# Optimization experiments

Hardware: AMD Instinct MI355X
Metric: run time of the kernel (lower is better)

Reference implementation:

```python
import jax, jax.numpy as jnp
import numpy as np

B, S, D, H = 4, 2048, 1024, 16
HD = D // H
ROPE_THETA = 10000.0


def setup_inputs() -> dict:
    key = jax.random.key(0)
    ks = jax.random.split(key, 5)
    scale = 1.0 / np.sqrt(D)
    inp = {
        "x": jax.random.normal(ks[0], (B, S, D), dtype=jnp.float32),
        "Wq": jax.random.normal(ks[1], (D, D), dtype=jnp.float32) * scale,
        "bq": jnp.zeros((D,), jnp.float32),
        "Wk": jax.random.normal(ks[2], (D, D), dtype=jnp.float32) * scale,
        "bk": jnp.zeros((D,), jnp.float32),
        "Wv": jax.random.normal(ks[3], (D, D), dtype=jnp.float32) * scale,
        "bv": jnp.zeros((D,), jnp.float32),
        "Wo": jax.random.normal(ks[4], (D, D), dtype=jnp.float32) * scale,
        "bo": jnp.zeros((D,), jnp.float32),
        # causal mask: True means masked (j > i), matching masked_fill semantics
        "attn_mask": jnp.triu(jnp.ones((S, S), dtype=bool), k=1),
    }
    return inp


def _rope(x):
    # x: [B, H, S, HD]; half-split rotary embedding
    half = HD // 2
    inv_freq = 1.0 / (ROPE_THETA ** (jnp.arange(0, half, dtype=jnp.float32) / half))
    pos = jnp.arange(x.shape[2], dtype=jnp.float32)
    freqs = pos[:, None] * inv_freq[None, :]            # [S, half]
    cos = jnp.cos(freqs)[None, None]                    # [1,1,S,half]
    sin = jnp.sin(freqs)[None, None]
    x1, x2 = x[..., :half], x[..., half:]
    return jnp.concatenate([x1 * cos - x2 * sin, x2 * cos + x1 * sin], axis=-1)


def reference(x, Wq, bq, Wk, bk, Wv, bv, Wo, bo, attn_mask):
    def shape(t):  # [B,S,D] -> [B,H,S,HD]
        return t.reshape(B, S, H, HD).transpose(0, 2, 1, 3)

    q = shape(x @ Wq.T + bq)
    k = shape(x @ Wk.T + bk)
    v = shape(x @ Wv.T + bv)
    q = _rope(q)
    k = _rope(k)
    scores = jnp.einsum("bhqd,bhkd->bhqk", q, k) * (HD ** -0.5)
    scores = jnp.where(attn_mask[None, None], -jnp.inf, scores)
    w = jax.nn.softmax(scores, axis=-1)
    attn = jnp.einsum("bhqk,bhkd->bhqd", w, v)
    merged = attn.transpose(0, 2, 1, 3).reshape(B, S, D)
    return merged @ Wo.T + bo
```

## Files before the change

### kernel.cpp

```cpp
#include <hip/hip_runtime.h>
#include <math.h>

#define BATCH 4
#define SEQ   2048
#define DMODEL 1024
#define NHEAD 16
#define HDIM  64
#define MROWS (BATCH*SEQ)

typedef unsigned short u16;
typedef unsigned int   u32;

using bf16x8 = __attribute__((ext_vector_type(8))) short;
using f32x4  = __attribute__((ext_vector_type(4))) float;
using f32x16 = __attribute__((ext_vector_type(16))) float;

__device__ __forceinline__ u16 f2bf(float f) {
    u32 u = __float_as_uint(f);
    u += 0x7fffu + ((u >> 16) & 1u);
    return (u16)(u >> 16);
}
__device__ __forceinline__ u32 pack2bf(float a, float b) {
    u32 ua = __float_as_uint(a); ua += 0x7fffu + ((ua >> 16) & 1u);
    u32 ub = __float_as_uint(b); ub += 0x7fffu + ((ub >> 16) & 1u);
    return (ua >> 16) | (ub & 0xffff0000u);
}

#define GLOBAL_LOAD_LDS16(gp, lp)                                              \
    __builtin_amdgcn_global_load_lds(                                          \
        (const __attribute__((address_space(1))) void*)(gp),                   \
        (__attribute__((address_space(3))) void*)(lp), 16, 0, 0)

__global__ __launch_bounds__(256) void convert_inputs(
    const float* __restrict__ x,  const float* __restrict__ wq,
    const float* __restrict__ wk, const float* __restrict__ wv,
    const float* __restrict__ wo, u16* __restrict__ dst)
{
    long long i4 = ((long long)blockIdx.x * 256 + threadIdx.x) * 4;
    const float* src; long long off;
    if (i4 < 8388608LL) { src = x; off = i4; }
    else {
        long long j = i4 - 8388608LL;
        int seg = (int)(j >> 20);
        off = j & 1048575LL;
        src = (seg == 0) ? wq : (seg == 1) ? wk : (seg == 2) ? wv : wo;
    }
    float4 v = *(const float4*)(src + off);
    u32 lo = (u32)f2bf(v.x) | ((u32)f2bf(v.y) << 16);
    u32 hi = (u32)f2bf(v.z) | ((u32)f2bf(v.w) << 16);
    *(uint2*)(dst + i4) = make_uint2(lo, hi);
}

template<int QKV>
__global__ __launch_bounds__(256) void gemm_mfma(
    const u16* __restrict__ A,
    const u16* __restrict__ Wq_, const u16* __restrict__ Wk_, const u16* __restrict__ Wv_,
    const float* __restrict__ bq_, const float* __restrict__ bk_, const float* __restrict__ bv_,
    u16* __restrict__ Cq_, u16* __restrict__ Ck_, u16* __restrict__ Cv_,
    float* __restrict__ Cf)
{
    __shared__ u16 As[128 * 32];
    __shared__ u16 Ws[128 * 32];

    const int t    = threadIdx.x;
    const int lane = t & 63;
    const int w    = t >> 6;
    const int quad = lane >> 4;
    const int l15  = lane & 15;

    const int bx  = blockIdx.x;
    const int xcd = bx & 7;
    const int i_  = bx >> 3;
    const int bml = i_ & 7;
    const int n_  = (QKV ? ((i_ >> 3) & 7) : (i_ >> 3));
    const int seg = (QKV ? (i_ >> 6) : 0);

    const u16*   W    = (seg == 0) ? Wq_ : (seg == 1) ? Wk_ : Wv_;
    const float* bias = (seg == 0) ? bq_ : (seg == 1) ? bk_ : bv_;
    u16*         Cb   = (seg == 0) ? Cq_ : (seg == 1) ? Ck_ : Cv_;

    const int bm   = (xcd * 8 + bml) * 128;
    const int bn   = n_ * 128;
    const int wrow = (w & 1) * 64;
    const int wcol = (w >> 1) * 64;

    const int srl = lane >> 2;
    const int sc  = (lane & 3) ^ ((lane >> 3) & 3);

    f32x4 acc[4][4] = {};

    for (int k0 = 0; k0 < DMODEL; k0 += 32) {
        __syncthreads();
        #pragma unroll
        for (int i = 0; i < 2; i++) {
            int row = 32 * w + 16 * i + srl;
            GLOBAL_LOAD_LDS16(A + (size_t)(bm + row) * DMODEL + k0 + sc * 8,
                              &As[(32 * w + 16 * i) * 32]);
            GLOBAL_LOAD_LDS16(W + (size_t)(bn + row) * DMODEL + k0 + sc * 8,
                              &Ws[(32 * w + 16 * i) * 32]);
        }
        __syncthreads();

        bf16x8 af[4], bfr[4];
        const int pc = quad ^ ((l15 >> 1) & 3);
        #pragma unroll
        for (int i = 0; i < 4; i++)
            af[i] = *(const bf16x8*)&As[(wrow + 16 * i + l15) * 32 + pc * 8];
        #pragma unroll
        for (int j = 0; j < 4; j++)
            bfr[j] = *(const bf16x8*)&Ws[(wcol + 16 * j + l15) * 32 + pc * 8];
        #pragma unroll
        for (int i = 0; i < 4; i++)
            #pragma unroll
            for (int j = 0; j < 4; j++)
                acc[i][j] = __builtin_amdgcn_mfma_f32_16x16x32_bf16(af[i], bfr[j], acc[i][j], 0, 0, 0);
    }

    float bv[4];
    #pragma unroll
    for (int j = 0; j < 4; j++) bv[j] = bias[bn + wcol + 16 * j + l15];

    if constexpr (QKV == 0) {
        #pragma unroll
        for (int i = 0; i < 4; i++)
            #pragma unroll
            for (int r = 0; r < 4; r++) {
                int mg = bm + wrow + 16 * i + quad * 4 + r;
                #pragma unroll
                for (int j = 0; j < 4; j++)
                    Cf[(size_t)mg * DMODEL + bn + wcol + 16 * j + l15] = acc[i][j][r] + bv[j];
            }
    } else {
        if (seg == 2) {
            #pragma unroll
            for (int i = 0; i < 4; i++)
                #pragma unroll
                for (int r = 0; r < 4; r++) {
                    int mg = bm + wrow + 16 * i + quad * 4 + r;
                    #pragma unroll
                    for (int j = 0; j < 4; j++)
                        Cb[(size_t)mg * DMODEL + bn + wcol + 16 * j + l15] = f2bf(acc[i][j][r] + bv[j]);
                }
        } else {
            const float qscale = (seg == 0) ? 0.125f : 1.0f;
            float inv[2];
            #pragma unroll
            for (int j = 0; j < 2; j++) {
                int d = 16 * j + l15;
                inv[j] = exp2f(-(float)d * 0.4152410118609203f);
            }
            #pragma unroll
            for (int i = 0; i < 4; i++)
                #pragma unroll
                for (int r = 0; r < 4; r++) {
                    int mg = bm + wrow + 16 * i + quad * 4 + r;
                    int s  = mg & (SEQ - 1);
                    #pragma unroll
                    for (int j = 0; j < 2; j++) {
                        float f = (float)s * inv[j];
                        float sn, cs;
                        __sincosf(f, &sn, &cs);
                        float a1 = acc[i][j][r]     + bv[j];
                        float a2 = acc[i][j + 2][r] + bv[j + 2];
                        float o1 = (a1 * cs - a2 * sn) * qscale;
                        float o2 = (a2 * cs + a1 * sn) * qscale;
                        Cb[(size_t)mg * DMODEL + bn + wcol + 16 * j       + l15] = f2bf(o1);
                        Cb[(size_t)mg * DMODEL + bn + wcol + 16 * (j + 2) + l15] = f2bf(o2);
                    }
                }
        }
    }
}

__global__ __launch_bounds__(256) void attn_mfma(
    const u16* __restrict__ Q, const u16* __restrict__ K,
    const u16* __restrict__ V, u16* __restrict__ O)
{
    __shared__ u16 Qs[128 * 64];
    __shared__ u16 Ks[64 * 64];
    __shared__ u16 Vt[64 * 64];
    __shared__ u16 Ps[128 * 64];
    __shared__ float lS[128];

    const int t    = threadIdx.x;
    const int lane = t & 63;
    const int w    = t >> 6;
    const int l31  = lane & 31;
    const int hl   = lane >> 5;
    const int bid  = blockIdx.x;
    const int bh   = bid & 63;
    const int qt   = 15 - (bid >> 6);
    const int h    = bh & (NHEAD - 1);
    const int b    = bh >> 4;
    const int q0   = qt * 128;

    const size_t gbase = ((size_t)b * SEQ) * DMODEL + h * HDIM;

    {
        int rl = lane >> 3, cp = lane & 7;
        int c  = cp ^ rl;
        #pragma unroll
        for (int i = 0; i < 4; i++) {
            int row = 32 * w + 8 * i + rl;
            GLOBAL_LOAD_LDS16(Q + gbase + (size_t)(q0 + row) * DMODEL + c * 8,
                              &Qs[(32 * w + 8 * i) * 64]);
        }
    }
    __syncthreads();

    bf16x8 qf[4];
    {
        int row = 32 * w + l31;
        #pragma unroll
        for (int s = 0; s < 4; s++) {
            int c = (hl + 2 * s) ^ (row & 7);
            qf[s] = *(const bf16x8*)&Qs[row * 64 + c * 8];
        }
    }

    float lsum = 0.0f;
    f32x16 oacc[2] = {};

    const int ktn = 2 * qt + 2;
    for (int kt = 0; kt < ktn; kt++) {
        const int k0 = kt * 64;
        __syncthreads();

        {
            int rl = lane >> 3, cp = lane & 7;
            int c  = cp ^ rl;
            #pragma unroll
            for (int i = 0; i < 2; i++) {
                int row = 16 * w + 8 * i + rl;
                GLOBAL_LOAD_LDS16(K + gbase + (size_t)(k0 + row) * DMODEL + c * 8,
                                  &Ks[(16 * w + 8 * i) * 64]);
            }
        }
        {
            int j0 = (t & 31) * 2, d0 = (t >> 5) * 8;
            uint4 va = *(const uint4*)(V + gbase + (size_t)(k0 + j0)     * DMODEL + d0);
            uint4 vb = *(const uint4*)(V + gbase + (size_t)(k0 + j0 + 1) * DMODEL + d0);
            const u16* pa = (const u16*)&va;
            const u16* pb = (const u16*)&vb;
            int jd = t & 31, pos = jd & 3, ch = jd >> 2;
            #pragma unroll
            for (int e = 0; e < 8; e++) {
                int row = d0 + e;
                int pcch = ch ^ (row & 7);
                *(u32*)&Vt[row * 64 + pcch * 8 + pos * 2] = (u32)pa[e] | ((u32)pb[e] << 16);
            }
        }
        __syncthreads();

        const bool act = (k0 <= q0 + 32 * w + 31);
        if (act) {
            const int qrow = 32 * w + l31;
            const int qg   = q0 + qrow;
            #pragma unroll
            for (int krh = 0; krh < 2; krh++) {
                const bool qact = (k0 + 32 * krh <= q0 + 32 * w + 31);
                if (!qact) {
                    #pragma unroll
                    for (int g = 0; g < 4; g++)
                        #pragma unroll
                        for (int pp = 0; pp < 2; pp++) {
                            int kr = 32 * krh + 8 * g + 4 * hl + 2 * pp;
                            int jd = kr >> 1;
                            int pcc = (jd >> 2) ^ (qrow & 7);
                            *(u32*)&Ps[qrow * 64 + pcc * 8 + (jd & 3) * 2] = 0u;
                        }
                    continue;
                }
                f32x16 s = {};
                #pragma unroll
                for (int stp = 0; stp < 4; stp++) {
                    int row = 32 * krh + l31;
                    int c   = (hl + 2 * stp) ^ (l31 & 7);
                    bf16x8 ka = *(const bf16x8*)&Ks[row * 64 + c * 8];
                    s = __builtin_amdgcn_mfma_f32_32x32x16_bf16(ka, qf[stp], s, 0, 0, 0);
                }
                if (k0 + 32 * krh + 31 > q0 + 32 * w) {
                    #pragma unroll
                    for (int r = 0; r < 16; r++) {
                        int krg = k0 + 32 * krh + (r & 3) + 8 * (r >> 2) + 4 * hl;
                        if (krg > qg) s[r] = -1e30f;
                    }
                }
                float pv[16];
                #pragma unroll
                for (int r = 0; r < 16; r++) { pv[r] = __expf(s[r]); lsum += pv[r]; }
                #pragma unroll
                for (int g = 0; g < 4; g++)
                    #pragma unroll
                    for (int pp = 0; pp < 2; pp++) {
                        int kr = 32 * krh + 8 * g + 4 * hl + 2 * pp;
                        int jd = kr >> 1;
                        int pcc = (jd >> 2) ^ (qrow & 7);
                        *(u32*)&Ps[qrow * 64 + pcc * 8 + (jd & 3) * 2] =
                            pack2bf(pv[4 * g + 2 * pp], pv[4 * g + 2 * pp + 1]);
                    }
            }

            #pragma unroll
            for (int stp = 0; stp < 4; stp++) {
                int c = (hl + 2 * stp) ^ (l31 & 7);
                bf16x8 pf = *(const bf16x8*)&Ps[qrow * 64 + c * 8];
                #pragma unroll
                for (int dh = 0; dh < 2; dh++) {
                    bf16x8 vf = *(const bf16x8*)&Vt[(32 * dh + l31) * 64 + c * 8];
                    oacc[dh] = __builtin_amdgcn_mfma_f32_32x32x16_bf16(pf, vf, oacc[dh], 0, 0, 0);
                }
            }
        }
    }

    lsum += __shfl_xor(lsum, 32, 64);
    if (lane < 32) lS[32 * w + lane] = lsum;
    __syncthreads();

    #pragma unroll
    for (int g = 0; g < 4; g++) {
        f32x4 lv = *(const f32x4*)&lS[32 * w + 8 * g + 4 * hl];
        #pragma unroll
        for (int rr = 0; rr < 4; rr++) {
            int qg = q0 + 32 * w + rr + 8 * g + 4 * hl;
            float inv = 1.0f / lv[rr];
            #pragma unroll
            for (int dh = 0; dh < 2; dh++) {
                float o = oacc[dh][4 * g + rr] * inv;
                O[gbase + (size_t)qg * DMODEL + 32 * dh + l31] = f2bf(o);
            }
        }
    }
}

extern "C" void kernel_launch(void* const* d_in, const int* in_sizes, int n_in,
                              void* d_out, int out_size, void* d_ws, size_t ws_size,
                              hipStream_t stream)
{
    const float* x  = (const float*)d_in[0];
    const float* Wq = (const float*)d_in[1];
    const float* bq = (const float*)d_in[2];
    const float* Wk = (const float*)d_in[3];
    const float* bk = (const float*)d_in[4];
    const float* Wv = (const float*)d_in[5];
    const float* bv = (const float*)d_in[6];
    const float* Wo = (const float*)d_in[7];
    const float* bo = (const float*)d_in[8];

    u16* wsp = (u16*)d_ws;
    u16* xb  = wsp;
    u16* Wqb = wsp + 8388608;
    u16* Wkb = Wqb + 1048576;
    u16* Wvb = Wkb + 1048576;
    u16* Wob = Wvb + 1048576;
    u16* Qb  = Wob + 1048576;
    u16* Kb  = Qb + 8388608;
    u16* Vb  = Kb + 8388608;
    u16* Ab  = Vb + 8388608;

    convert_inputs<<<12288, 256, 0, stream>>>(x, Wq, Wk, Wv, Wo, xb);

    gemm_mfma<1><<<1536, 256, 0, stream>>>(xb, Wqb, Wkb, Wvb, bq, bk, bv,
                                           Qb, Kb, Vb, nullptr);

    attn_mfma<<<1024, 256, 0, stream>>>(Qb, Kb, Vb, Ab);

    gemm_mfma<0><<<512, 256, 0, stream>>>(Ab, Wob, nullptr, nullptr, bo, nullptr, nullptr,
                                          nullptr, nullptr, nullptr, (float*)d_out);
}
```

Before: 280.0 us.

## Shrink attention LDS via register P shuffles, split output GEMM into smaller tiles

```diff
diff --git a/kernel.cpp b/kernel.cpp
--- a/kernel.cpp
+++ b/kernel.cpp
@@ -51,13 +51,11 @@
     *(uint2*)(dst + i4) = make_uint2(lo, hi);
 }
 
-template<int QKV>
-__global__ __launch_bounds__(256) void gemm_mfma(
+__global__ __launch_bounds__(256) void gemm_qkv(
     const u16* __restrict__ A,
     const u16* __restrict__ Wq_, const u16* __restrict__ Wk_, const u16* __restrict__ Wv_,
     const float* __restrict__ bq_, const float* __restrict__ bk_, const float* __restrict__ bv_,
-    u16* __restrict__ Cq_, u16* __restrict__ Ck_, u16* __restrict__ Cv_,
-    float* __restrict__ Cf)
+    u16* __restrict__ Cq_, u16* __restrict__ Ck_, u16* __restrict__ Cv_)
 {
     __shared__ u16 As[128 * 32];
     __shared__ u16 Ws[128 * 32];
@@ -72,8 +70,8 @@
     const int xcd = bx & 7;
     const int i_  = bx >> 3;
     const int bml = i_ & 7;
-    const int n_  = (QKV ? ((i_ >> 3) & 7) : (i_ >> 3));
-    const int seg = (QKV ? (i_ >> 6) : 0);
+    const int n_  = (i_ >> 3) & 7;
+    const int seg = i_ >> 6;
 
     const u16*   W    = (seg == 0) ? Wq_ : (seg == 1) ? Wk_ : Wv_;
     const float* bias = (seg == 0) ? bq_ : (seg == 1) ? bk_ : bv_;
@@ -120,7 +118,7 @@
     #pragma unroll
     for (int j = 0; j < 4; j++) bv[j] = bias[bn + wcol + 16 * j + l15];
 
-    if constexpr (QKV == 0) {
+    if (seg == 2) {
         #pragma unroll
         for (int i = 0; i < 4; i++)
             #pragma unroll
@@ -128,59 +126,116 @@
                 int mg = bm + wrow + 16 * i + quad * 4 + r;
                 #pragma unroll
                 for (int j = 0; j < 4; j++)
-                    Cf[(size_t)mg * DMODEL + bn + wcol + 16 * j + l15] = acc[i][j][r] + bv[j];
+                    Cb[(size_t)mg * DMODEL + bn + wcol + 16 * j + l15] = f2bf(acc[i][j][r] + bv[j]);
             }
     } else {
-        if (seg == 2) {
-            #pragma unroll
-            for (int i = 0; i < 4; i++)
+        const float qscale = (seg == 0) ? 0.18033688011112042f : 1.0f;
+        float inv[2];
+        #pragma unroll
+        for (int j = 0; j < 2; j++) {
+            int d = 16 * j + l15;
+            inv[j] = exp2f(-(float)d * 0.4152410118609203f);
+        }
+        #pragma unroll
+        for (int i = 0; i < 4; i++)
+            #pragma unroll
+            for (int r = 0; r < 4; r++) {
+                int mg = bm + wrow + 16 * i + quad * 4 + r;
+                int s  = mg & (SEQ - 1);
                 #pragma unroll
-                for (int r = 0; r < 4; r++) {
-                    int mg = bm + wrow + 16 * i + quad * 4 + r;
-                    #pragma unroll
-                    for (int j = 0; j < 4; j++)
-                        Cb[(size_t)mg * DMODEL + bn + wcol + 16 * j + l15] = f2bf(acc[i][j][r] + bv[j]);
+                for (int j = 0; j < 2; j++) {
+                    float f = (float)s * inv[j];
+                    float sn, cs;
+                    __sincosf(f, &sn, &cs);
+                    float a1 = acc[i][j][r]     + bv[j];
+                    float a2 = acc[i][j + 2][r] + bv[j + 2];
+                    float o1 = (a1 * cs - a2 * sn) * qscale;
+                    float o2 = (a2 * cs + a1 * sn) * qscale;
+                    Cb[(size_t)mg * DMODEL + bn + wcol + 16 * j       + l15] = f2bf(o1);
+                    Cb[(size_t)mg * DMODEL + bn + wcol + 16 * (j + 2) + l15] = f2bf(o2);
                 }
-        } else {
-            const float qscale = (seg == 0) ? 0.125f : 1.0f;
-            float inv[2];
-            #pragma unroll
-            for (int j = 0; j < 2; j++) {
-                int d = 16 * j + l15;
-                inv[j] = exp2f(-(float)d * 0.4152410118609203f);
-            }
-            #pragma unroll
-            for (int i = 0; i < 4; i++)
-                #pragma unroll
-                for (int r = 0; r < 4; r++) {
-                    int mg = bm + wrow + 16 * i + quad * 4 + r;
-                    int s  = mg & (SEQ - 1);
-                    #pragma unroll
-                    for (int j = 0; j < 2; j++) {
-                        float f = (float)s * inv[j];
-                        float sn, cs;
-                        __sincosf(f, &sn, &cs);
-                        float a1 = acc[i][j][r]     + bv[j];
-                        float a2 = acc[i][j + 2][r] + bv[j + 2];
-                        float o1 = (a1 * cs - a2 * sn) * qscale;
-                        float o2 = (a2 * cs + a1 * sn) * qscale;
-                        Cb[(size_t)mg * DMODEL + bn + wcol + 16 * j       + l15] = f2bf(o1);
-                        Cb[(size_t)mg * DMODEL + bn + wcol + 16 * (j + 2) + l15] = f2bf(o2);
-                    }
-                }
-        }
-    }
-}
-
-__global__ __launch_bounds__(256) void attn_mfma(
+            }
+    }
+}
+
+__global__ __launch_bounds__(256) void gemm_out(
+    const u16* __restrict__ A, const u16* __restrict__ W,
+    const float* __restrict__ bias, float* __restrict__ C)
+{
+    __shared__ u16 As[64 * 32];
+    __shared__ u16 Ws[128 * 32];
+
+    const int t    = threadIdx.x;
+    const int lane = t & 63;
+    const int w    = t >> 6;
+    const int quad = lane >> 4;
+    const int l15  = lane & 15;
+
+    const int bx  = blockIdx.x;
+    const int xcd = bx & 7;
+    const int i_  = bx >> 3;
+    const int bml = i_ & 15;
+    const int n_  = i_ >> 4;
+
+    const int bm   = (xcd * 16 + bml) * 64;
+    const int bn   = n_ * 128;
+    const int wrow = (w & 1) * 32;
+    const int wcol = (w >> 1) * 64;
+
+    const int srl = lane >> 2;
+    const int sc  = (lane & 3) ^ ((lane >> 3) & 3);
+
+    f32x4 acc[2][4] = {};
+
+    for (int k0 = 0; k0 < DMODEL; k0 += 32) {
+        __syncthreads();
+        GLOBAL_LOAD_LDS16(A + (size_t)(bm + 16 * w + srl) * DMODEL + k0 + sc * 8,
+                          &As[(16 * w) * 32]);
+        #pragma unroll
+        for (int i = 0; i < 2; i++) {
+            int row = 32 * w + 16 * i + srl;
+            GLOBAL_LOAD_LDS16(W + (size_t)(bn + row) * DMODEL + k0 + sc * 8,
+                              &Ws[(32 * w + 16 * i) * 32]);
+        }
+        __syncthreads();
+
+        bf16x8 af[2], bfr[4];
+        const int pc = quad ^ ((l15 >> 1) & 3);
+        #pragma unroll
+        for (int i = 0; i < 2; i++)
+            af[i] = *(const bf16x8*)&As[(wrow + 16 * i + l15) * 32 + pc * 8];
+        #pragma unroll
+        for (int j = 0; j < 4; j++)
+            bfr[j] = *(const bf16x8*)&Ws[(wcol + 16 * j + l15) * 32 + pc * 8];
+        #pragma unroll
+        for (int i = 0; i < 2; i++)
+            #pragma unroll
+            for (int j = 0; j < 4; j++)
+                acc[i][j] = __builtin_amdgcn_mfma_f32_16x16x32_bf16(af[i], bfr[j], acc[i][j], 0, 0, 0);
+    }
+
+    float bv[4];
+    #pragma unroll
+    for (int j = 0; j < 4; j++) bv[j] = bias[bn + wcol + 16 * j + l15];
+    #pragma unroll
+    for (int i = 0; i < 2; i++)
+        #pragma unroll
+        for (int r = 0; r < 4; r++) {
+            int mg = bm + wrow + 16 * i + quad * 4 + r;
+            #pragma unroll
+            for (int j = 0; j < 4; j++)
+                C[(size_t)mg * DMODEL + bn + wcol + 16 * j + l15] = acc[i][j][r] + bv[j];
+        }
+}
+
+__global__ __launch_bounds__(256, 4) void attn_mfma(
     const u16* __restrict__ Q, const u16* __restrict__ K,
     const u16* __restrict__ V, u16* __restrict__ O)
 {
     __shared__ u16 Qs[128 * 64];
-    __shared__ u16 Ks[64 * 64];
-    __shared__ u16 Vt[64 * 64];
-    __shared__ u16 Ps[128 * 64];
     __shared__ float lS[128];
+    u16* const Ks = Qs;
+    u16* const Vt = Qs + 64 * 64;
 
     const int t    = threadIdx.x;
     const int lane = t & 63;
@@ -196,27 +251,26 @@
 
     const size_t gbase = ((size_t)b * SEQ) * DMODEL + h * HDIM;
 
-    {
-        int rl = lane >> 3, cp = lane & 7;
-        int c  = cp ^ rl;
-        #pragma unroll
-        for (int i = 0; i < 4; i++) {
-            int row = 32 * w + 8 * i + rl;
-            GLOBAL_LOAD_LDS16(Q + gbase + (size_t)(q0 + row) * DMODEL + c * 8,
-                              &Qs[(32 * w + 8 * i) * 64]);
-        }
+    const int rl = lane >> 3, cp = lane & 7;
+
+    #pragma unroll
+    for (int i = 0; i < 4; i++) {
+        int row = 32 * w + 8 * i + rl;
+        int c   = cp ^ rl ^ ((4 * w + i) & 7);
+        GLOBAL_LOAD_LDS16(Q + gbase + (size_t)(q0 + row) * DMODEL + c * 8,
+                          &Qs[(32 * w + 8 * i) * 64]);
     }
     __syncthreads();
 
+    const int qrow = 32 * w + l31;
+    const int qg   = q0 + qrow;
     bf16x8 qf[4];
-    {
-        int row = 32 * w + l31;
-        #pragma unroll
-        for (int s = 0; s < 4; s++) {
-            int c = (hl + 2 * s) ^ (row & 7);
-            qf[s] = *(const bf16x8*)&Qs[row * 64 + c * 8];
-        }
-    }
+    #pragma unroll
+    for (int s = 0; s < 4; s++) {
+        int c = (hl + 2 * s) ^ ((qrow ^ (qrow >> 3)) & 7);
+        qf[s] = *(const bf16x8*)&Qs[qrow * 64 + c * 8];
+    }
+    __syncthreads();
 
     float lsum = 0.0f;
     f32x16 oacc[2] = {};
@@ -224,98 +278,87 @@
     const int ktn = 2 * qt + 2;
     for (int kt = 0; kt < ktn; kt++) {
         const int k0 = kt * 64;
-        __syncthreads();
-
+
+        #pragma unroll
+        for (int i = 0; i < 2; i++) {
+            int row = 16 * w + 8 * i + rl;
+            int c   = cp ^ rl ^ ((2 * w + i) & 7);
+            GLOBAL_LOAD_LDS16(K + gbase + (size_t)(k0 + row) * DMODEL + c * 8,
+                              &Ks[(16 * w + 8 * i) * 64]);
+        }
         {
-            int rl = lane >> 3, cp = lane & 7;
-            int c  = cp ^ rl;
-            #pragma unroll
-            for (int i = 0; i < 2; i++) {
-                int row = 16 * w + 8 * i + rl;
-                GLOBAL_LOAD_LDS16(K + gbase + (size_t)(k0 + row) * DMODEL + c * 8,
-                                  &Ks[(16 * w + 8 * i) * 64]);
-            }
-        }
-        {
-            int j0 = (t & 31) * 2, d0 = (t >> 5) * 8;
-            uint4 va = *(const uint4*)(V + gbase + (size_t)(k0 + j0)     * DMODEL + d0);
-            uint4 vb = *(const uint4*)(V + gbase + (size_t)(k0 + j0 + 1) * DMODEL + d0);
+            int u = t >> 3, v = t & 7;
+            int j0 = 2 * u;
+            uint4 va = *(const uint4*)(V + gbase + (size_t)(k0 + j0)     * DMODEL + 8 * v);
+            uint4 vb = *(const uint4*)(V + gbase + (size_t)(k0 + j0 + 1) * DMODEL + 8 * v);
             const u16* pa = (const u16*)&va;
             const u16* pb = (const u16*)&vb;
-            int jd = t & 31, pos = jd & 3, ch = jd >> 2;
             #pragma unroll
             for (int e = 0; e < 8; e++) {
-                int row = d0 + e;
-                int pcch = ch ^ (row & 7);
-                *(u32*)&Vt[row * 64 + pcch * 8 + pos * 2] = (u32)pa[e] | ((u32)pb[e] << 16);
-            }
-        }
-        __syncthreads();
-
-        const bool act = (k0 <= q0 + 32 * w + 31);
-        if (act) {
-            const int qrow = 32 * w + l31;
-            const int qg   = q0 + qrow;
-            #pragma unroll
-            for (int krh = 0; krh < 2; krh++) {
-                const bool qact = (k0 + 32 * krh <= q0 + 32 * w + 31);
-                if (!qact) {
-                    #pragma unroll
-                    for (int g = 0; g < 4; g++)
-                        #pragma unroll
-                        for (int pp = 0; pp < 2; pp++) {
-                            int kr = 32 * krh + 8 * g + 4 * hl + 2 * pp;
-                            int jd = kr >> 1;
-                            int pcc = (jd >> 2) ^ (qrow & 7);
-                            *(u32*)&Ps[qrow * 64 + pcc * 8 + (jd & 3) * 2] = 0u;
-                        }
-                    continue;
+                int row = 8 * v + e;
+                int pch = (u >> 2) ^ e ^ v;
+                *(u32*)&Vt[row * 64 + pch * 8 + (u & 3) * 2] =
+                    (u32)pa[e] | ((u32)pb[e] << 16);
+            }
+        }
+        __syncthreads();
+
+        #pragma unroll
+        for (int krh = 0; krh < 2; krh++) {
+            const int kcb = k0 + 32 * krh;
+            if (kcb > q0 + 32 * w + 31) continue;
+
+            f32x16 s = {};
+            #pragma unroll
+            for (int stp = 0; stp < 4; stp++) {
+                int row = 32 * krh + l31;
+                int c   = (hl + 2 * stp) ^ ((row ^ (row >> 3)) & 7);
+                bf16x8 ka = *(const bf16x8*)&Ks[row * 64 + c * 8];
+                s = __builtin_amdgcn_mfma_f32_32x32x16_bf16(ka, qf[stp], s, 0, 0, 0);
+            }
+            if (kcb + 31 > q0 + 32 * w) {
+                #pragma unroll
+                for (int r = 0; r < 16; r++) {
+                    int krg = kcb + (r & 3) + 8 * (r >> 2) + 4 * hl;
+                    if (krg > qg) s[r] = -1e30f;
                 }
-                f32x16 s = {};
+            }
+            float pv[16];
+            #pragma unroll
+            for (int r = 0; r < 16; r++) { pv[r] = exp2f(s[r]); lsum += pv[r]; }
+            u32 pr[4][2];
+            #pragma unroll
+            for (int rho = 0; rho < 4; rho++)
                 #pragma unroll
-                for (int stp = 0; stp < 4; stp++) {
-                    int row = 32 * krh + l31;
-                    int c   = (hl + 2 * stp) ^ (l31 & 7);
-                    bf16x8 ka = *(const bf16x8*)&Ks[row * 64 + c * 8];
-                    s = __builtin_amdgcn_mfma_f32_32x32x16_bf16(ka, qf[stp], s, 0, 0, 0);
-                }
-                if (k0 + 32 * krh + 31 > q0 + 32 * w) {
-                    #pragma unroll
-                    for (int r = 0; r < 16; r++) {
-                        int krg = k0 + 32 * krh + (r & 3) + 8 * (r >> 2) + 4 * hl;
-                        if (krg > qg) s[r] = -1e30f;
-                    }
-                }
-                float pv[16];
-                #pragma unroll
-                for (int r = 0; r < 16; r++) { pv[r] = __expf(s[r]); lsum += pv[r]; }
-                #pragma unroll
-                for (int g = 0; g < 4; g++)
-                    #pragma unroll
-                    for (int pp = 0; pp < 2; pp++) {
-                        int kr = 32 * krh + 8 * g + 4 * hl + 2 * pp;
-                        int jd = kr >> 1;
-                        int pcc = (jd >> 2) ^ (qrow & 7);
-                        *(u32*)&Ps[qrow * 64 + pcc * 8 + (jd & 3) * 2] =
-                            pack2bf(pv[4 * g + 2 * pp], pv[4 * g + 2 * pp + 1]);
-                    }
-            }
-
-            #pragma unroll
-            for (int stp = 0; stp < 4; stp++) {
-                int c = (hl + 2 * stp) ^ (l31 & 7);
-                bf16x8 pf = *(const bf16x8*)&Ps[qrow * 64 + c * 8];
+                for (int p = 0; p < 2; p++)
+                    pr[rho][p] = pack2bf(pv[4 * rho + 2 * p], pv[4 * rho + 2 * p + 1]);
+
+            #pragma unroll
+            for (int sh = 0; sh < 2; sh++) {
+                int sg = 2 * krh + sh;
+                u32 self0 = pr[2 * sh + hl][0],        self1 = pr[2 * sh + hl][1];
+                u32 pub0  = pr[2 * sh + (hl ^ 1)][0],  pub1  = pr[2 * sh + (hl ^ 1)][1];
+                u32 got0 = (u32)__shfl_xor((int)pub0, 32, 64);
+                u32 got1 = (u32)__shfl_xor((int)pub1, 32, 64);
+                union { u32 u[4]; bf16x8 v; } pf;
+                pf.u[0] = hl ? got0 : self0;
+                pf.u[1] = hl ? got1 : self1;
+                pf.u[2] = hl ? self0 : got0;
+                pf.u[3] = hl ? self1 : got1;
                 #pragma unroll
                 for (int dh = 0; dh < 2; dh++) {
-                    bf16x8 vf = *(const bf16x8*)&Vt[(32 * dh + l31) * 64 + c * 8];
-                    oacc[dh] = __builtin_amdgcn_mfma_f32_32x32x16_bf16(pf, vf, oacc[dh], 0, 0, 0);
+                    int vrow = 32 * dh + l31;
+                    int c    = (hl + 2 * sg) ^ ((vrow ^ (vrow >> 3)) & 7);
+                    bf16x8 vf = *(const bf16x8*)&Vt[vrow * 64 + c * 8];
+                    oacc[dh] = __builtin_amdgcn_mfma_f32_32x32x16_bf16(pf.v, vf, oacc[dh], 0, 0, 0);
                 }
             }
         }
+        __syncthreads();
     }
 
     lsum += __shfl_xor(lsum, 32, 64);
-    if (lane < 32) lS[32 * w + lane] = lsum;
+    if (hl == 0) lS[32 * w + l31] = lsum;
     __syncthreads();
 
     #pragma unroll
@@ -323,12 +366,12 @@
         f32x4 lv = *(const f32x4*)&lS[32 * w + 8 * g + 4 * hl];
         #pragma unroll
         for (int rr = 0; rr < 4; rr++) {
-            int qg = q0 + 32 * w + rr + 8 * g + 4 * hl;
+            int qgw = q0 + 32 * w + rr + 8 * g + 4 * hl;
             float inv = 1.0f / lv[rr];
             #pragma unroll
             for (int dh = 0; dh < 2; dh++) {
                 float o = oacc[dh][4 * g + rr] * inv;
-                O[gbase + (size_t)qg * DMODEL + 32 * dh + l31] = f2bf(o);
+                O[gbase + (size_t)qgw * DMODEL + 32 * dh + l31] = f2bf(o);
             }
         }
     }
@@ -361,11 +404,9 @@
 
     convert_inputs<<<12288, 256, 0, stream>>>(x, Wq, Wk, Wv, Wo, xb);
 
-    gemm_mfma<1><<<1536, 256, 0, stream>>>(xb, Wqb, Wkb, Wvb, bq, bk, bv,
-                                           Qb, Kb, Vb, nullptr);
+    gemm_qkv<<<1536, 256, 0, stream>>>(xb, Wqb, Wkb, Wvb, bq, bk, bv, Qb, Kb, Vb);
 
     attn_mfma<<<1024, 256, 0, stream>>>(Qb, Kb, Vb, Ab);
 
-    gemm_mfma<0><<<512, 256, 0, stream>>>(Ab, Wob, nullptr, nullptr, bo, nullptr, nullptr,
-                                          nullptr, nullptr, nullptr, (float*)d_out);
-}
+    gemm_out<<<1024, 256, 0, stream>>>(Ab, Wob, bo, (float*)d_out);
+}
```

After: 308.6 us. +10.2%, slower.
